# Optimization experiments

Measured on AMD Instinct MI355X. Metric: run time of the kernel, lower is better.

## Reference

```python
import jax, jax.numpy as jnp
import numpy as np

N = 50000      # nodes
E = 800000     # edges
H = 64         # hid_dim (== in_dim)
T = 4          # number of S2V message-passing steps


def setup_inputs() -> dict:
    key = jax.random.key(0)
    ks = jax.random.split(key, 12)
    mu = jax.random.normal(ks[0], (N, H), dtype=jnp.float32)
    x = jax.random.uniform(ks[1], (N, 1), dtype=jnp.float32)
    edge_index = jax.random.randint(ks[2], (2, E), 0, N, dtype=jnp.int64)
    edge_w = jax.random.uniform(ks[3], (E, 1), dtype=jnp.float32)
    s = 0.05  # small init scale to keep activations bounded across T relu layers
    W1 = jax.random.normal(ks[4], (T, H, 1), dtype=jnp.float32) * s   # lin1 per layer, torch [out,in]
    W2 = jax.random.normal(ks[5], (T, H, H), dtype=jnp.float32) * s   # lin2 per layer
    W3 = jax.random.normal(ks[6], (T, H, H), dtype=jnp.float32) * s   # lin3 per layer
    W4 = jax.random.normal(ks[7], (T, H, 1), dtype=jnp.float32) * s   # lin4 per layer
    W5 = jax.random.normal(ks[8], (1, 2 * H), dtype=jnp.float32) * s  # lin5
    W7 = jax.random.normal(ks[9], (H, H), dtype=jnp.float32) * s      # lin7
    return {"mu": mu, "x": x, "edge_index": edge_index, "edge_w": edge_w,
            "W1": W1, "W2": W2, "W3": W3, "W4": W4, "W5": W5, "W7": W7}


def _s2v_step(mu, x, idx, edge_w, w1, w2, w3, w4):
    # Faithful to source: gather AND scatter both use edge_index[1].
    x_emb = x @ w1.T                                            # [N,H]
    mu_j = mu[idx]                                              # [E,H] gather
    mu_aggr = jax.ops.segment_sum(mu_j, idx, num_segments=N)    # [N,H] scatter_add
    mu_aggr = mu_aggr @ w2.T
    ew = jax.nn.relu(edge_w @ w4.T)                             # [E,H]
    ew_aggr = jax.ops.segment_sum(ew, idx, num_segments=N)      # [N,H]
    ew_aggr = ew_aggr @ w3.T
    return jax.nn.relu(x_emb + mu_aggr + ew_aggr)


def reference(mu, x, edge_index, edge_w, W1, W2, W3, W4, W5, W7):
    idx = edge_index[1]
    for t in range(T):
        mu = _s2v_step(mu, x, idx, edge_w, W1[t], W2[t], W3[t], W4[t])
    nodes_vec = mu @ W7.T                                       # [N,H]
    graph_pool = jnp.broadcast_to(jnp.sum(mu, axis=0, keepdims=True), (N, H))
    cat = jnp.concatenate([graph_pool, nodes_vec], axis=1)      # [N,2H]
    return (jax.nn.relu(cat) @ W5.T).squeeze(-1)                # [N]
```

## Files before the change

kernel.cpp:

```cpp
#include <hip/hip_runtime.h>

#define H 64
#define NPB 64
#define KS 104
typedef short bf16x8 __attribute__((ext_vector_type(8)));
typedef float f32x4 __attribute__((ext_vector_type(4)));

static __device__ __forceinline__ unsigned short f2bf(float f) {
    union { float f; unsigned u; } v; v.f = f;
    unsigned r = v.u + 0x7fffu + ((v.u >> 16) & 1u);
    return (unsigned short)(r >> 16);
}
static __device__ __forceinline__ float bf2f(unsigned short b) {
    union { unsigned u; float f; } v; v.u = ((unsigned)b) << 16;
    return v.f;
}
static __device__ __forceinline__ void split8(const float* ff, bf16x8& hi, bf16x8& lo) {
#pragma unroll
    for (int j = 0; j < 8; ++j) {
        unsigned short h = f2bf(ff[j]);
        hi[j] = (short)h;
        lo[j] = (short)f2bf(ff[j] - bf2f(h));
    }
}


__global__ __launch_bounds__(256)
void prep_kernel(const float* __restrict__ W1, const float* __restrict__ W2,
                 const float* __restrict__ W3, const float* __restrict__ W4,
                 const float* __restrict__ W7, unsigned* __restrict__ zero_base,
                 int zero_dwords, bf16x8* __restrict__ Bp, bf16x8* __restrict__ W7p) {
    const int t = threadIdx.x;
    if (blockIdx.x != 0) {
        int idx = (blockIdx.x - 1) * 256 + t;
        for (int i = idx; i < zero_dwords; i += 64 * 256) zero_base[i] = 0u;
        return;
    }
    __shared__ float v3s[4 * H];
    {
        int tl = t >> 6, h = t & 63;
        const float* __restrict__ w3r = W3 + (tl * H + h) * H;
        const float* __restrict__ w4r = W4 + tl * H;
        float a0 = 0, a1 = 0, a2 = 0, a3 = 0;
#pragma unroll
        for (int k = 0; k < H; k += 4) {
            a0 += fmaxf(w4r[k + 0], 0.f) * w3r[k + 0];
            a1 += fmaxf(w4r[k + 1], 0.f) * w3r[k + 1];
            a2 += fmaxf(w4r[k + 2], 0.f) * w3r[k + 2];
            a3 += fmaxf(w4r[k + 3], 0.f) * w3r[k + 3];
        }
        v3s[t] = (a0 + a1) + (a2 + a3);
    }
    __syncthreads();
    const int w = t >> 6, lane = t & 63, c = lane & 15, q = lane >> 4;
    const int hh = 16 * w + c;
    for (int tl = 0; tl < 4; ++tl) {
        const int b3 = (tl * 4 + w) * 3;
        bf16x8 hi, lo;
#pragma unroll
        for (int s = 0; s < 2; ++s) {
            const float* __restrict__ wp = W2 + (tl * H + hh) * H + s * 32 + q * 8;
            float4 f0 = *(const float4*)(wp);
            float4 f1 = *(const float4*)(wp + 4);
            float ff[8] = {f0.x, f0.y, f0.z, f0.w, f1.x, f1.y, f1.z, f1.w};
            split8(ff, hi, lo);
            Bp[(b3 + s) * 128 + lane] = hi;
            Bp[(b3 + s) * 128 + 64 + lane] = lo;
        }
        float ff[8] = {0, 0, 0, 0, 0, 0, 0, 0};
        if (q == 0) { ff[0] = W1[tl * H + hh]; ff[1] = v3s[tl * H + hh]; }
        split8(ff, hi, lo);
        Bp[(b3 + 2) * 128 + lane] = hi;
        Bp[(b3 + 2) * 128 + 64 + lane] = lo;
    }
#pragma unroll
    for (int s = 0; s < 2; ++s) {
        const float* __restrict__ wp = W7 + hh * H + s * 32 + q * 8;
        float4 f0 = *(const float4*)(wp);
        float4 f1 = *(const float4*)(wp + 4);
        float ff[8] = {f0.x, f0.y, f0.z, f0.w, f1.x, f1.y, f1.z, f1.w};
        bf16x8 hi, lo;
        split8(ff, hi, lo);
        W7p[(w * 2 + s) * 128 + lane] = hi;
        W7p[(w * 2 + s) * 128 + 64 + lane] = lo;
    }
}

__global__ __launch_bounds__(256)
void edge_kernel(const int* __restrict__ ei, const float* __restrict__ ew,
                 double* __restrict__ dS, int E) {
    int probe = ei[2 * (threadIdx.x & 63) + 1];
    bool is64 = (__ballot(probe != 0) == 0ULL);
    int e0 = 4 * (blockIdx.x * blockDim.x + threadIdx.x);
    if (e0 >= E) return;
    if (e0 + 3 < E) {
        float4 wv = *(const float4*)(ew + e0);
        int i0, i1, i2, i3;
        if (is64) {
            int4 a = *(const int4*)(ei + 2 * (E + e0));
            int4 b = *(const int4*)(ei + 2 * (E + e0) + 4);
            i0 = a.x; i1 = a.z; i2 = b.x; i3 = b.z;
        } else {
            int4 a = *(const int4*)(ei + E + e0);
            i0 = a.x; i1 = a.y; i2 = a.z; i3 = a.w;
        }
        unsafeAtomicAdd(&dS[i0], 4096.0 + (double)wv.x);
        unsafeAtomicAdd(&dS[i1], 4096.0 + (double)wv.y);
        unsafeAtomicAdd(&dS[i2], 4096.0 + (double)wv.z);
        unsafeAtomicAdd(&dS[i3], 4096.0 + (double)wv.w);
    } else {
        for (int j = 0; j < 4 && e0 + j < E; ++j) {
            int e = e0 + j;
            int idx = is64 ? ei[2 * (E + e)] : ei[E + e];
            unsafeAtomicAdd(&dS[idx], 4096.0 + (double)ew[e]);
        }
    }
}

__global__ __launch_bounds__(256, 2)
void node_kernel(const float* __restrict__ mu, const float* __restrict__ x,
                 const float* __restrict__ W5, const bf16x8* __restrict__ Bp,
                 const bf16x8* __restrict__ W7p, const double* __restrict__ dS,
                 float* __restrict__ gp, float* __restrict__ out, int N) {
    __shared__ unsigned short Ab[2][NPB * KS];
    __shared__ float degs[NPB];
    __shared__ float red[4 * NPB];

    const int t = threadIdx.x;
    const int lane = t & 63;
    const int w = __builtin_amdgcn_readfirstlane(t >> 6);
    const int c = lane & 15;
    const int q = lane >> 4;
    const int hh = 16 * w + c;
    const int base = blockIdx.x * NPB;

    if (t < 128) {
        int buf = t >> 6, row = t & 63;
        unsigned* p = (unsigned*)&Ab[buf][row * KS];
#pragma unroll
        for (int d = 33; d < 52; ++d) p[d] = 0u;
    }
    if (t < 64) {
        int node = base + t;
        float dg = 0.f, sv = 0.f, xv = 0.f;
        if (node < N) {
            double T = dS[node];
            double k = floor(T * (1.0 / 4096.0));
            dg = (float)k;
            sv = (float)(T - 4096.0 * k);
            xv = x[node];
        }
        degs[t] = dg;
        unsigned short xb = f2bf(xv), sb = f2bf(sv);
        Ab[0][t * KS + 64] = xb; Ab[0][t * KS + 65] = sb;
        Ab[1][t * KS + 64] = xb; Ab[1][t * KS + 65] = sb;
    }
    __syncthreads();

    {
        const float* __restrict__ mublk = mu + (size_t)base * H;
        const int maxf = (N - base) * H;
#pragma unroll
        for (int cc = 0; cc < 4; ++cc) {
            int f = (t + 256 * cc) * 4;
            float4 v = make_float4(0.f, 0.f, 0.f, 0.f);
            if (f < maxf) v = *(const float4*)(mublk + f);
            int m = f >> 6, k = f & 63;
            float dg = degs[m];
            ushort4 b;
            b.x = f2bf(v.x * dg); b.y = f2bf(v.y * dg);
            b.z = f2bf(v.z * dg); b.w = f2bf(v.w * dg);
            *(ushort4*)(&Ab[0][m * KS + k]) = b;
        }
    }
    __syncthreads();

    unsigned short* Acur = &Ab[0][0];
    unsigned short* Anxt = &Ab[1][0];

    for (int tl = 0; tl < 4; ++tl) {
        const int b3 = (tl * 4 + w) * 3;
        bf16x8 bh0 = Bp[(b3 + 0) * 128 + lane], bl0 = Bp[(b3 + 0) * 128 + 64 + lane];
        bf16x8 bh1 = Bp[(b3 + 1) * 128 + lane], bl1 = Bp[(b3 + 1) * 128 + 64 + lane];
        bf16x8 bh2 = Bp[(b3 + 2) * 128 + lane], bl2 = Bp[(b3 + 2) * 128 + 64 + lane];

        f32x4 acc[4];
#pragma unroll
        for (int mt = 0; mt < 4; ++mt)
#pragma unroll
            for (int r = 0; r < 4; ++r) acc[mt][r] = 0.f;

#pragma unroll
        for (int mt = 0; mt < 4; ++mt) {
            const unsigned short* ar = Acur + (mt * 16 + c) * KS;
            bf16x8 a0 = *(const bf16x8*)(ar + q * 8);
            bf16x8 a1 = *(const bf16x8*)(ar + 32 + q * 8);
            bf16x8 a2 = *(const bf16x8*)(ar + 64 + q * 8);
            acc[mt] = __builtin_amdgcn_mfma_f32_16x16x32_bf16(a0, bh0, acc[mt], 0, 0, 0);
            acc[mt] = __builtin_amdgcn_mfma_f32_16x16x32_bf16(a0, bl0, acc[mt], 0, 0, 0);
            acc[mt] = __builtin_amdgcn_mfma_f32_16x16x32_bf16(a1, bh1, acc[mt], 0, 0, 0);
            acc[mt] = __builtin_amdgcn_mfma_f32_16x16x32_bf16(a1, bl1, acc[mt], 0, 0, 0);
            acc[mt] = __builtin_amdgcn_mfma_f32_16x16x32_bf16(a2, bh2, acc[mt], 0, 0, 0);
            acc[mt] = __builtin_amdgcn_mfma_f32_16x16x32_bf16(a2, bl2, acc[mt], 0, 0, 0);
        }

        const bool scale = (tl < 3);
#pragma unroll
        for (int mt = 0; mt < 4; ++mt) {
#pragma unroll
            for (int r = 0; r < 4; ++r) {
                int m = mt * 16 + q * 4 + r;
                float v = fmaxf(acc[mt][r], 0.f);
                if (scale) v *= degs[m];
                Anxt[m * KS + hh] = f2bf(v);
            }
        }
        __syncthreads();
        unsigned short* tmp = Acur; Acur = Anxt; Anxt = tmp;
    }

    {
        bf16x8 bh0 = W7p[(w * 2 + 0) * 128 + lane], bl0 = W7p[(w * 2 + 0) * 128 + 64 + lane];
        bf16x8 bh1 = W7p[(w * 2 + 1) * 128 + lane], bl1 = W7p[(w * 2 + 1) * 128 + 64 + lane];
        f32x4 acc[4];
#pragma unroll
        for (int mt = 0; mt < 4; ++mt)
#pragma unroll
            for (int r = 0; r < 4; ++r) acc[mt][r] = 0.f;
#pragma unroll
        for (int mt = 0; mt < 4; ++mt) {
            const unsigned short* ar = Acur + (mt * 16 + c) * KS;
            bf16x8 a0 = *(const bf16x8*)(ar + q * 8);
            bf16x8 a1 = *(const bf16x8*)(ar + 32 + q * 8);
            acc[mt] = __builtin_amdgcn_mfma_f32_16x16x32_bf16(a0, bh0, acc[mt], 0, 0, 0);
            acc[mt] = __builtin_amdgcn_mfma_f32_16x16x32_bf16(a0, bl0, acc[mt], 0, 0, 0);
            acc[mt] = __builtin_amdgcn_mfma_f32_16x16x32_bf16(a1, bh1, acc[mt], 0, 0, 0);
            acc[mt] = __builtin_amdgcn_mfma_f32_16x16x32_bf16(a1, bl1, acc[mt], 0, 0, 0);
        }
        float w5v = W5[H + hh];
#pragma unroll
        for (int mt = 0; mt < 4; ++mt) {
#pragma unroll
            for (int r = 0; r < 4; ++r) {
                float v = fmaxf(acc[mt][r], 0.f) * w5v;
                v += __shfl_xor(v, 1);
                v += __shfl_xor(v, 2);
                v += __shfl_xor(v, 4);
                v += __shfl_xor(v, 8);
                if (c == 0) red[w * 64 + mt * 16 + q * 4 + r] = v;
            }
        }
    }
    __syncthreads();
    if (t < 64) {
        float pn = red[t] + red[64 + t] + red[128 + t] + red[192 + t];
        if (base + t < N) out[base + t] = pn;
    }
    __syncthreads();

    {
        int h = t & 63, mq = t >> 6;
        float s = 0.f;
#pragma unroll
        for (int i = 0; i < 16; ++i) s += bf2f(Acur[(mq * 16 + i) * KS + h]);
        red[t] = s;
    }
    __syncthreads();
    if (t < 64) {
        float g = red[t] + red[64 + t] + red[128 + t] + red[192 + t];
        unsafeAtomicAdd(&gp[t], g);
    }
}

__global__ __launch_bounds__(256)
void finalize_kernel(const float* __restrict__ gp, const float* __restrict__ W5,
                     float* __restrict__ out, int N) {
    int lane = threadIdx.x & 63;
    float v = fmaxf(gp[lane], 0.f) * W5[lane];
    v += __shfl_xor(v, 1);
    v += __shfl_xor(v, 2);
    v += __shfl_xor(v, 4);
    v += __shfl_xor(v, 8);
    v += __shfl_xor(v, 16);
    v += __shfl_xor(v, 32);
    int n = blockIdx.x * blockDim.x + threadIdx.x;
    if (n < N) out[n] += v;
}

extern "C" void kernel_launch(void* const* d_in, const int* in_sizes, int n_in,
                              void* d_out, int out_size, void* d_ws, size_t ws_size,
                              hipStream_t stream) {
    const float* mu = (const float*)d_in[0];
    const float* x  = (const float*)d_in[1];
    const int*   ei = (const int*)d_in[2];
    const float* ew = (const float*)d_in[3];
    const float* W1 = (const float*)d_in[4];
    const float* W2 = (const float*)d_in[5];
    const float* W3 = (const float*)d_in[6];
    const float* W4 = (const float*)d_in[7];
    const float* W5 = (const float*)d_in[8];
    const float* W7 = (const float*)d_in[9];
    float* out = (float*)d_out;

    const int N = in_sizes[1];
    const int E = in_sizes[3];

    char* ws = (char*)d_ws;
    double* dS  = (double*)ws;
    float*  gp  = (float*)(ws + (size_t)N * 8);
    bf16x8* Bp  = (bf16x8*)(ws + (size_t)N * 8 + 256);
    bf16x8* W7p = (bf16x8*)(ws + (size_t)N * 8 + 256 + 196608);
    int zero_dwords = N * 2 + 64;

    prep_kernel<<<65, 256, 0, stream>>>(W1, W2, W3, W4, W7, (unsigned*)dS,
                                        zero_dwords, Bp, W7p);
    edge_kernel<<<(E + 1023) / 1024, 256, 0, stream>>>(ei, ew, dS, E);
    node_kernel<<<(N + NPB - 1) / NPB, 256, 0, stream>>>(mu, x, W5, Bp, W7p,
                                                         dS, gp, out, N);
    finalize_kernel<<<(N + 255) / 256, 256, 0, stream>>>(gp, W5, out, N);
}
```

Measured before the change: 150.2 us.

## Fuse prep, edge, node and finalize kernels into one cooperative persistent kernel

Replaces the four-kernel launch sequence with a single cooperative kernel that uses grid-wide syncs between phases: zeroing, weight packing plus edge atomics, persistent node-tile processing, and the final graph-pool add. The grid is sized from occupancy and capped at 768 blocks, and blocks loop over node tiles. This removes three launch boundaries and their inter-kernel gaps. In exchange it adds grid.sync overhead, reserves one block for weight prep during the edge phase, and depends on the cooperative-launch occupancy being valid at launch_bounds(256,3).

```diff
diff --git a/kernel.cpp b/kernel.cpp
--- a/kernel.cpp
+++ b/kernel.cpp
@@ -1,4 +1,6 @@
 #include <hip/hip_runtime.h>
+#include <hip/hip_cooperative_groups.h>
+namespace cg = cooperative_groups;
 
 #define H 64
 #define NPB 64
@@ -24,115 +26,114 @@
     }
 }
 
-
-__global__ __launch_bounds__(256)
-void prep_kernel(const float* __restrict__ W1, const float* __restrict__ W2,
-                 const float* __restrict__ W3, const float* __restrict__ W4,
-                 const float* __restrict__ W7, unsigned* __restrict__ zero_base,
-                 int zero_dwords, bf16x8* __restrict__ Bp, bf16x8* __restrict__ W7p) {
-    const int t = threadIdx.x;
-    if (blockIdx.x != 0) {
-        int idx = (blockIdx.x - 1) * 256 + t;
-        for (int i = idx; i < zero_dwords; i += 64 * 256) zero_base[i] = 0u;
-        return;
-    }
-    __shared__ float v3s[4 * H];
-    {
-        int tl = t >> 6, h = t & 63;
-        const float* __restrict__ w3r = W3 + (tl * H + h) * H;
-        const float* __restrict__ w4r = W4 + tl * H;
-        float a0 = 0, a1 = 0, a2 = 0, a3 = 0;
-#pragma unroll
-        for (int k = 0; k < H; k += 4) {
-            a0 += fmaxf(w4r[k + 0], 0.f) * w3r[k + 0];
-            a1 += fmaxf(w4r[k + 1], 0.f) * w3r[k + 1];
-            a2 += fmaxf(w4r[k + 2], 0.f) * w3r[k + 2];
-            a3 += fmaxf(w4r[k + 3], 0.f) * w3r[k + 3];
-        }
-        v3s[t] = (a0 + a1) + (a2 + a3);
-    }
-    __syncthreads();
-    const int w = t >> 6, lane = t & 63, c = lane & 15, q = lane >> 4;
-    const int hh = 16 * w + c;
-    for (int tl = 0; tl < 4; ++tl) {
-        const int b3 = (tl * 4 + w) * 3;
-        bf16x8 hi, lo;
-#pragma unroll
-        for (int s = 0; s < 2; ++s) {
-            const float* __restrict__ wp = W2 + (tl * H + hh) * H + s * 32 + q * 8;
-            float4 f0 = *(const float4*)(wp);
-            float4 f1 = *(const float4*)(wp + 4);
-            float ff[8] = {f0.x, f0.y, f0.z, f0.w, f1.x, f1.y, f1.z, f1.w};
-            split8(ff, hi, lo);
-            Bp[(b3 + s) * 128 + lane] = hi;
-            Bp[(b3 + s) * 128 + 64 + lane] = lo;
-        }
-        float ff[8] = {0, 0, 0, 0, 0, 0, 0, 0};
-        if (q == 0) { ff[0] = W1[tl * H + hh]; ff[1] = v3s[tl * H + hh]; }
-        split8(ff, hi, lo);
-        Bp[(b3 + 2) * 128 + lane] = hi;
-        Bp[(b3 + 2) * 128 + 64 + lane] = lo;
-    }
-#pragma unroll
-    for (int s = 0; s < 2; ++s) {
-        const float* __restrict__ wp = W7 + hh * H + s * 32 + q * 8;
-        float4 f0 = *(const float4*)(wp);
-        float4 f1 = *(const float4*)(wp + 4);
-        float ff[8] = {f0.x, f0.y, f0.z, f0.w, f1.x, f1.y, f1.z, f1.w};
-        bf16x8 hi, lo;
-        split8(ff, hi, lo);
-        W7p[(w * 2 + s) * 128 + lane] = hi;
-        W7p[(w * 2 + s) * 128 + 64 + lane] = lo;
-    }
-}
-
-__global__ __launch_bounds__(256)
-void edge_kernel(const int* __restrict__ ei, const float* __restrict__ ew,
-                 double* __restrict__ dS, int E) {
-    int probe = ei[2 * (threadIdx.x & 63) + 1];
-    bool is64 = (__ballot(probe != 0) == 0ULL);
-    int e0 = 4 * (blockIdx.x * blockDim.x + threadIdx.x);
-    if (e0 >= E) return;
-    if (e0 + 3 < E) {
-        float4 wv = *(const float4*)(ew + e0);
-        int i0, i1, i2, i3;
-        if (is64) {
-            int4 a = *(const int4*)(ei + 2 * (E + e0));
-            int4 b = *(const int4*)(ei + 2 * (E + e0) + 4);
-            i0 = a.x; i1 = a.z; i2 = b.x; i3 = b.z;
-        } else {
-            int4 a = *(const int4*)(ei + E + e0);
-            i0 = a.x; i1 = a.y; i2 = a.z; i3 = a.w;
-        }
-        unsafeAtomicAdd(&dS[i0], 4096.0 + (double)wv.x);
-        unsafeAtomicAdd(&dS[i1], 4096.0 + (double)wv.y);
-        unsafeAtomicAdd(&dS[i2], 4096.0 + (double)wv.z);
-        unsafeAtomicAdd(&dS[i3], 4096.0 + (double)wv.w);
-    } else {
-        for (int j = 0; j < 4 && e0 + j < E; ++j) {
-            int e = e0 + j;
-            int idx = is64 ? ei[2 * (E + e)] : ei[E + e];
-            unsafeAtomicAdd(&dS[idx], 4096.0 + (double)ew[e]);
-        }
-    }
-}
-
-__global__ __launch_bounds__(256, 2)
-void node_kernel(const float* __restrict__ mu, const float* __restrict__ x,
-                 const float* __restrict__ W5, const bf16x8* __restrict__ Bp,
-                 const bf16x8* __restrict__ W7p, const double* __restrict__ dS,
-                 float* __restrict__ gp, float* __restrict__ out, int N) {
+__global__ __launch_bounds__(256, 3)
+void fused_kernel(const float* __restrict__ mu, const float* __restrict__ x,
+                  const int* __restrict__ ei, const float* __restrict__ ew,
+                  const float* __restrict__ W1, const float* __restrict__ W2,
+                  const float* __restrict__ W3, const float* __restrict__ W4,
+                  const float* __restrict__ W5, const float* __restrict__ W7,
+                  double* __restrict__ dS, float* __restrict__ gp,
+                  bf16x8* __restrict__ Bp, bf16x8* __restrict__ W7p,
+                  float* __restrict__ out, int N, int E) {
+    cg::grid_group grid = cg::this_grid();
     __shared__ unsigned short Ab[2][NPB * KS];
     __shared__ float degs[NPB];
-    __shared__ float red[4 * NPB];
+    __shared__ float red[256];
+    __shared__ float v3s[256];
 
     const int t = threadIdx.x;
+    const int bid = blockIdx.x;
+    const int nb = gridDim.x;
     const int lane = t & 63;
     const int w = __builtin_amdgcn_readfirstlane(t >> 6);
     const int c = lane & 15;
     const int q = lane >> 4;
     const int hh = 16 * w + c;
-    const int base = blockIdx.x * NPB;
+
+    {
+        unsigned* zb = (unsigned*)dS;
+        const int zd = 2 * N;
+        for (int i = bid * 256 + t; i < zd; i += nb * 256) zb[i] = 0u;
+        if (bid == 0 && t < 64) gp[t] = 0.f;
+    }
+    grid.sync();
+
+    if (bid == 0) {
+        {
+            int tl = t >> 6, h2 = t & 63;
+            const float* __restrict__ w3r = W3 + (tl * H + h2) * H;
+            const float* __restrict__ w4r = W4 + tl * H;
+            float a0 = 0, a1 = 0, a2 = 0, a3 = 0;
+#pragma unroll
+            for (int k = 0; k < H; k += 4) {
+                a0 += fmaxf(w4r[k + 0], 0.f) * w3r[k + 0];
+                a1 += fmaxf(w4r[k + 1], 0.f) * w3r[k + 1];
+                a2 += fmaxf(w4r[k + 2], 0.f) * w3r[k + 2];
+                a3 += fmaxf(w4r[k + 3], 0.f) * w3r[k + 3];
+            }
+            v3s[t] = (a0 + a1) + (a2 + a3);
+        }
+        __syncthreads();
+        for (int tl = 0; tl < 4; ++tl) {
+            const int b3 = (tl * 4 + w) * 3;
+            bf16x8 hi, lo;
+#pragma unroll
+            for (int s = 0; s < 2; ++s) {
+                const float* __restrict__ wp = W2 + (tl * H + hh) * H + s * 32 + q * 8;
+                float4 f0 = *(const float4*)(wp);
+                float4 f1 = *(const float4*)(wp + 4);
+                float ff[8] = {f0.x, f0.y, f0.z, f0.w, f1.x, f1.y, f1.z, f1.w};
+                split8(ff, hi, lo);
+                Bp[(b3 + s) * 128 + lane] = hi;
+                Bp[(b3 + s) * 128 + 64 + lane] = lo;
+            }
+            float ff[8] = {0, 0, 0, 0, 0, 0, 0, 0};
+            if (q == 0) { ff[0] = W1[tl * H + hh]; ff[1] = v3s[tl * H + hh]; }
+            split8(ff, hi, lo);
+            Bp[(b3 + 2) * 128 + lane] = hi;
+            Bp[(b3 + 2) * 128 + 64 + lane] = lo;
+        }
+#pragma unroll
+        for (int s = 0; s < 2; ++s) {
+            const float* __restrict__ wp = W7 + hh * H + s * 32 + q * 8;
+            float4 f0 = *(const float4*)(wp);
+            float4 f1 = *(const float4*)(wp + 4);
+            float ff[8] = {f0.x, f0.y, f0.z, f0.w, f1.x, f1.y, f1.z, f1.w};
+            bf16x8 hi, lo;
+            split8(ff, hi, lo);
+            W7p[(w * 2 + s) * 128 + lane] = hi;
+            W7p[(w * 2 + s) * 128 + 64 + lane] = lo;
+        }
+    } else {
+        int probe = ei[2 * (t & 63) + 1];
+        bool is64 = (__ballot(probe != 0) == 0ULL);
+        const int nth = (nb - 1) * 256;
+        for (int e0 = 4 * ((bid - 1) * 256 + t); e0 < E; e0 += 4 * nth) {
+            if (e0 + 3 < E) {
+                float4 wv = *(const float4*)(ew + e0);
+                int i0, i1, i2, i3;
+                if (is64) {
+                    int4 a = *(const int4*)(ei + 2 * (E + e0));
+                    int4 b = *(const int4*)(ei + 2 * (E + e0) + 4);
+                    i0 = a.x; i1 = a.z; i2 = b.x; i3 = b.z;
+                } else {
+                    int4 a = *(const int4*)(ei + E + e0);
+                    i0 = a.x; i1 = a.y; i2 = a.z; i3 = a.w;
+                }
+                unsafeAtomicAdd(&dS[i0], 4096.0 + (double)wv.x);
+                unsafeAtomicAdd(&dS[i1], 4096.0 + (double)wv.y);
+                unsafeAtomicAdd(&dS[i2], 4096.0 + (double)wv.z);
+                unsafeAtomicAdd(&dS[i3], 4096.0 + (double)wv.w);
+            } else {
+                for (int j = 0; j < 4 && e0 + j < E; ++j) {
+                    int e = e0 + j;
+                    int idx = is64 ? ei[2 * (E + e)] : ei[E + e];
+                    unsafeAtomicAdd(&dS[idx], 4096.0 + (double)ew[e]);
+                }
+            }
+        }
+    }
+    grid.sync();
 
     if (t < 128) {
         int buf = t >> 6, row = t & 63;
@@ -140,151 +141,154 @@
 #pragma unroll
         for (int d = 33; d < 52; ++d) p[d] = 0u;
     }
-    if (t < 64) {
-        int node = base + t;
-        float dg = 0.f, sv = 0.f, xv = 0.f;
-        if (node < N) {
-            double T = dS[node];
-            double k = floor(T * (1.0 / 4096.0));
-            dg = (float)k;
-            sv = (float)(T - 4096.0 * k);
-            xv = x[node];
-        }
-        degs[t] = dg;
-        unsigned short xb = f2bf(xv), sb = f2bf(sv);
-        Ab[0][t * KS + 64] = xb; Ab[0][t * KS + 65] = sb;
-        Ab[1][t * KS + 64] = xb; Ab[1][t * KS + 65] = sb;
-    }
-    __syncthreads();
+    const int ntiles = (N + NPB - 1) / NPB;
+    for (int tile = bid; tile < ntiles; tile += nb) {
+        const int base = tile * NPB;
+
+        if (t < 64) {
+            int node = base + t;
+            float dg = 0.f, sv = 0.f, xv = 0.f;
+            if (node < N) {
+                double T = dS[node];
+                double k = floor(T * (1.0 / 4096.0));
+                dg = (float)k;
+                sv = (float)(T - 4096.0 * k);
+                xv = x[node];
+            }
+            degs[t] = dg;
+            unsigned short xb = f2bf(xv), sb = f2bf(sv);
+            Ab[0][t * KS + 64] = xb; Ab[0][t * KS + 65] = sb;
+            Ab[1][t * KS + 64] = xb; Ab[1][t * KS + 65] = sb;
+        }
+        __syncthreads();
+
+        {
+            const float* __restrict__ mublk = mu + (size_t)base * H;
+            const int maxf = (N - base) * H;
+#pragma unroll
+            for (int cc = 0; cc < 4; ++cc) {
+                int f = (t + 256 * cc) * 4;
+                float4 v = make_float4(0.f, 0.f, 0.f, 0.f);
+                if (f < maxf) v = *(const float4*)(mublk + f);
+                int m = f >> 6, k = f & 63;
+                float dg = degs[m];
+                ushort4 b;
+                b.x = f2bf(v.x * dg); b.y = f2bf(v.y * dg);
+                b.z = f2bf(v.z * dg); b.w = f2bf(v.w * dg);
+                *(ushort4*)(&Ab[0][m * KS + k]) = b;
+            }
+        }
+        __syncthreads();
+
+        unsigned short* Acur = &Ab[0][0];
+        unsigned short* Anxt = &Ab[1][0];
+
+        for (int tl = 0; tl < 4; ++tl) {
+            const int b3 = (tl * 4 + w) * 3;
+            bf16x8 bh0 = Bp[(b3 + 0) * 128 + lane], bl0 = Bp[(b3 + 0) * 128 + 64 + lane];
+            bf16x8 bh1 = Bp[(b3 + 1) * 128 + lane], bl1 = Bp[(b3 + 1) * 128 + 64 + lane];
+            bf16x8 bh2 = Bp[(b3 + 2) * 128 + lane], bl2 = Bp[(b3 + 2) * 128 + 64 + lane];
+
+            f32x4 acc[4];
+#pragma unroll
+            for (int mt = 0; mt < 4; ++mt)
+#pragma unroll
+                for (int r = 0; r < 4; ++r) acc[mt][r] = 0.f;
+
+#pragma unroll
+            for (int mt = 0; mt < 4; ++mt) {
+                const unsigned short* ar = Acur + (mt * 16 + c) * KS;
+                bf16x8 a0 = *(const bf16x8*)(ar + q * 8);
+                bf16x8 a1 = *(const bf16x8*)(ar + 32 + q * 8);
+                bf16x8 a2 = *(const bf16x8*)(ar + 64 + q * 8);
+                acc[mt] = __builtin_amdgcn_mfma_f32_16x16x32_bf16(a0, bh0, acc[mt], 0, 0, 0);
+                acc[mt] = __builtin_amdgcn_mfma_f32_16x16x32_bf16(a0, bl0, acc[mt], 0, 0, 0);
+                acc[mt] = __builtin_amdgcn_mfma_f32_16x16x32_bf16(a1, bh1, acc[mt], 0, 0, 0);
+                acc[mt] = __builtin_amdgcn_mfma_f32_16x16x32_bf16(a1, bl1, acc[mt], 0, 0, 0);
+                acc[mt] = __builtin_amdgcn_mfma_f32_16x16x32_bf16(a2, bh2, acc[mt], 0, 0, 0);
+                acc[mt] = __builtin_amdgcn_mfma_f32_16x16x32_bf16(a2, bl2, acc[mt], 0, 0, 0);
+            }
+
+            const bool scale = (tl < 3);
+#pragma unroll
+            for (int mt = 0; mt < 4; ++mt) {
+#pragma unroll
+                for (int r = 0; r < 4; ++r) {
+                    int m = mt * 16 + q * 4 + r;
+                    float v = fmaxf(acc[mt][r], 0.f);
+                    if (scale) v *= degs[m];
+                    Anxt[m * KS + hh] = f2bf(v);
+                }
+            }
+            __syncthreads();
+            unsigned short* tmp = Acur; Acur = Anxt; Anxt = tmp;
+        }
+
+        {
+            bf16x8 bh0 = W7p[(w * 2 + 0) * 128 + lane], bl0 = W7p[(w * 2 + 0) * 128 + 64 + lane];
+            bf16x8 bh1 = W7p[(w * 2 + 1) * 128 + lane], bl1 = W7p[(w * 2 + 1) * 128 + 64 + lane];
+            f32x4 acc[4];
+#pragma unroll
+            for (int mt = 0; mt < 4; ++mt)
+#pragma unroll
+                for (int r = 0; r < 4; ++r) acc[mt][r] = 0.f;
+#pragma unroll
+            for (int mt = 0; mt < 4; ++mt) {
+                const unsigned short* ar = Acur + (mt * 16 + c) * KS;
+                bf16x8 a0 = *(const bf16x8*)(ar + q * 8);
+                bf16x8 a1 = *(const bf16x8*)(ar + 32 + q * 8);
+                acc[mt] = __builtin_amdgcn_mfma_f32_16x16x32_bf16(a0, bh0, acc[mt], 0, 0, 0);
+                acc[mt] = __builtin_amdgcn_mfma_f32_16x16x32_bf16(a0, bl0, acc[mt], 0, 0, 0);
+                acc[mt] = __builtin_amdgcn_mfma_f32_16x16x32_bf16(a1, bh1, acc[mt], 0, 0, 0);
+                acc[mt] = __builtin_amdgcn_mfma_f32_16x16x32_bf16(a1, bl1, acc[mt], 0, 0, 0);
+            }
+            float w5v = W5[H + hh];
+#pragma unroll
+            for (int mt = 0; mt < 4; ++mt) {
+#pragma unroll
+                for (int r = 0; r < 4; ++r) {
+                    float v = fmaxf(acc[mt][r], 0.f) * w5v;
+                    v += __shfl_xor(v, 1);
+                    v += __shfl_xor(v, 2);
+                    v += __shfl_xor(v, 4);
+                    v += __shfl_xor(v, 8);
+                    if (c == 0) red[w * 64 + mt * 16 + q * 4 + r] = v;
+                }
+            }
+        }
+        __syncthreads();
+        if (t < 64) {
+            float pn = red[t] + red[64 + t] + red[128 + t] + red[192 + t];
+            if (base + t < N) out[base + t] = pn;
+        }
+        __syncthreads();
+
+        {
+            int h2 = t & 63, mq = t >> 6;
+            float s = 0.f;
+#pragma unroll
+            for (int i = 0; i < 16; ++i) s += bf2f(Acur[(mq * 16 + i) * KS + h2]);
+            red[t] = s;
+        }
+        __syncthreads();
+        if (t < 64) {
+            float g = red[t] + red[64 + t] + red[128 + t] + red[192 + t];
+            unsafeAtomicAdd(&gp[t], g);
+        }
+        __syncthreads();
+    }
+    grid.sync();
 
     {
-        const float* __restrict__ mublk = mu + (size_t)base * H;
-        const int maxf = (N - base) * H;
-#pragma unroll
-        for (int cc = 0; cc < 4; ++cc) {
-            int f = (t + 256 * cc) * 4;
-            float4 v = make_float4(0.f, 0.f, 0.f, 0.f);
-            if (f < maxf) v = *(const float4*)(mublk + f);
-            int m = f >> 6, k = f & 63;
-            float dg = degs[m];
-            ushort4 b;
-            b.x = f2bf(v.x * dg); b.y = f2bf(v.y * dg);
-            b.z = f2bf(v.z * dg); b.w = f2bf(v.w * dg);
-            *(ushort4*)(&Ab[0][m * KS + k]) = b;
-        }
-    }
-    __syncthreads();
-
-    unsigned short* Acur = &Ab[0][0];
-    unsigned short* Anxt = &Ab[1][0];
-
-    for (int tl = 0; tl < 4; ++tl) {
-        const int b3 = (tl * 4 + w) * 3;
-        bf16x8 bh0 = Bp[(b3 + 0) * 128 + lane], bl0 = Bp[(b3 + 0) * 128 + 64 + lane];
-        bf16x8 bh1 = Bp[(b3 + 1) * 128 + lane], bl1 = Bp[(b3 + 1) * 128 + 64 + lane];
-        bf16x8 bh2 = Bp[(b3 + 2) * 128 + lane], bl2 = Bp[(b3 + 2) * 128 + 64 + lane];
-
-        f32x4 acc[4];
-#pragma unroll
-        for (int mt = 0; mt < 4; ++mt)
-#pragma unroll
-            for (int r = 0; r < 4; ++r) acc[mt][r] = 0.f;
-
-#pragma unroll
-        for (int mt = 0; mt < 4; ++mt) {
-            const unsigned short* ar = Acur + (mt * 16 + c) * KS;
-            bf16x8 a0 = *(const bf16x8*)(ar + q * 8);
-            bf16x8 a1 = *(const bf16x8*)(ar + 32 + q * 8);
-            bf16x8 a2 = *(const bf16x8*)(ar + 64 + q * 8);
-            acc[mt] = __builtin_amdgcn_mfma_f32_16x16x32_bf16(a0, bh0, acc[mt], 0, 0, 0);
-            acc[mt] = __builtin_amdgcn_mfma_f32_16x16x32_bf16(a0, bl0, acc[mt], 0, 0, 0);
-            acc[mt] = __builtin_amdgcn_mfma_f32_16x16x32_bf16(a1, bh1, acc[mt], 0, 0, 0);
-            acc[mt] = __builtin_amdgcn_mfma_f32_16x16x32_bf16(a1, bl1, acc[mt], 0, 0, 0);
-            acc[mt] = __builtin_amdgcn_mfma_f32_16x16x32_bf16(a2, bh2, acc[mt], 0, 0, 0);
-            acc[mt] = __builtin_amdgcn_mfma_f32_16x16x32_bf16(a2, bl2, acc[mt], 0, 0, 0);
-        }
-
-        const bool scale = (tl < 3);
-#pragma unroll
-        for (int mt = 0; mt < 4; ++mt) {
-#pragma unroll
-            for (int r = 0; r < 4; ++r) {
-                int m = mt * 16 + q * 4 + r;
-                float v = fmaxf(acc[mt][r], 0.f);
-                if (scale) v *= degs[m];
-                Anxt[m * KS + hh] = f2bf(v);
-            }
-        }
-        __syncthreads();
-        unsigned short* tmp = Acur; Acur = Anxt; Anxt = tmp;
-    }
-
-    {
-        bf16x8 bh0 = W7p[(w * 2 + 0) * 128 + lane], bl0 = W7p[(w * 2 + 0) * 128 + 64 + lane];
-        bf16x8 bh1 = W7p[(w * 2 + 1) * 128 + lane], bl1 = W7p[(w * 2 + 1) * 128 + 64 + lane];
-        f32x4 acc[4];
-#pragma unroll
-        for (int mt = 0; mt < 4; ++mt)
-#pragma unroll
-            for (int r = 0; r < 4; ++r) acc[mt][r] = 0.f;
-#pragma unroll
-        for (int mt = 0; mt < 4; ++mt) {
-            const unsigned short* ar = Acur + (mt * 16 + c) * KS;
-            bf16x8 a0 = *(const bf16x8*)(ar + q * 8);
-            bf16x8 a1 = *(const bf16x8*)(ar + 32 + q * 8);
-            acc[mt] = __builtin_amdgcn_mfma_f32_16x16x32_bf16(a0, bh0, acc[mt], 0, 0, 0);
-            acc[mt] = __builtin_amdgcn_mfma_f32_16x16x32_bf16(a0, bl0, acc[mt], 0, 0, 0);
-            acc[mt] = __builtin_amdgcn_mfma_f32_16x16x32_bf16(a1, bh1, acc[mt], 0, 0, 0);
-            acc[mt] = __builtin_amdgcn_mfma_f32_16x16x32_bf16(a1, bl1, acc[mt], 0, 0, 0);
-        }
-        float w5v = W5[H + hh];
-#pragma unroll
-        for (int mt = 0; mt < 4; ++mt) {
-#pragma unroll
-            for (int r = 0; r < 4; ++r) {
-                float v = fmaxf(acc[mt][r], 0.f) * w5v;
-                v += __shfl_xor(v, 1);
-                v += __shfl_xor(v, 2);
-                v += __shfl_xor(v, 4);
-                v += __shfl_xor(v, 8);
-                if (c == 0) red[w * 64 + mt * 16 + q * 4 + r] = v;
-            }
-        }
-    }
-    __syncthreads();
-    if (t < 64) {
-        float pn = red[t] + red[64 + t] + red[128 + t] + red[192 + t];
-        if (base + t < N) out[base + t] = pn;
-    }
-    __syncthreads();
-
-    {
-        int h = t & 63, mq = t >> 6;
-        float s = 0.f;
-#pragma unroll
-        for (int i = 0; i < 16; ++i) s += bf2f(Acur[(mq * 16 + i) * KS + h]);
-        red[t] = s;
-    }
-    __syncthreads();
-    if (t < 64) {
-        float g = red[t] + red[64 + t] + red[128 + t] + red[192 + t];
-        unsafeAtomicAdd(&gp[t], g);
-    }
-}
-
-__global__ __launch_bounds__(256)
-void finalize_kernel(const float* __restrict__ gp, const float* __restrict__ W5,
-                     float* __restrict__ out, int N) {
-    int lane = threadIdx.x & 63;
-    float v = fmaxf(gp[lane], 0.f) * W5[lane];
-    v += __shfl_xor(v, 1);
-    v += __shfl_xor(v, 2);
-    v += __shfl_xor(v, 4);
-    v += __shfl_xor(v, 8);
-    v += __shfl_xor(v, 16);
-    v += __shfl_xor(v, 32);
-    int n = blockIdx.x * blockDim.x + threadIdx.x;
-    if (n < N) out[n] += v;
+        float v = fmaxf(gp[lane], 0.f) * W5[lane];
+        v += __shfl_xor(v, 1);
+        v += __shfl_xor(v, 2);
+        v += __shfl_xor(v, 4);
+        v += __shfl_xor(v, 8);
+        v += __shfl_xor(v, 16);
+        v += __shfl_xor(v, 32);
+        for (int n = bid * 256 + t; n < N; n += nb * 256) out[n] += v;
+    }
 }
 
 extern "C" void kernel_launch(void* const* d_in, const int* in_sizes, int n_in,
@@ -302,20 +306,23 @@
     const float* W7 = (const float*)d_in[9];
     float* out = (float*)d_out;
 
-    const int N = in_sizes[1];
-    const int E = in_sizes[3];
+    int N = in_sizes[1];
+    int E = in_sizes[3];
 
     char* ws = (char*)d_ws;
     double* dS  = (double*)ws;
     float*  gp  = (float*)(ws + (size_t)N * 8);
     bf16x8* Bp  = (bf16x8*)(ws + (size_t)N * 8 + 256);
     bf16x8* W7p = (bf16x8*)(ws + (size_t)N * 8 + 256 + 196608);
-    int zero_dwords = N * 2 + 64;
-
-    prep_kernel<<<65, 256, 0, stream>>>(W1, W2, W3, W4, W7, (unsigned*)dS,
-                                        zero_dwords, Bp, W7p);
-    edge_kernel<<<(E + 1023) / 1024, 256, 0, stream>>>(ei, ew, dS, E);
-    node_kernel<<<(N + NPB - 1) / NPB, 256, 0, stream>>>(mu, x, W5, Bp, W7p,
-                                                         dS, gp, out, N);
-    finalize_kernel<<<(N + 255) / 256, 256, 0, stream>>>(gp, W5, out, N);
-}
+
+    int maxb = 0;
+    hipOccupancyMaxActiveBlocksPerMultiprocessor(&maxb, fused_kernel, 256, 0);
+    if (maxb < 1) maxb = 1;
+    int nb = maxb * 256;
+    if (nb > 768) nb = 768;
+
+    void* args[] = {&mu, &x, &ei, &ew, &W1, &W2, &W3, &W4, &W5, &W7,
+                    &dS, &gp, &Bp, &W7p, &out, &N, &E};
+    hipLaunchCooperativeKernel((void*)fused_kernel, dim3(nb), dim3(256),
+                               args, 0, stream);
+}
```

Measured after the change: 289.8 us. 92.9% more time.

## Merge weight prep into edge kernel and pack degree/weight sums in fp32

Applied to the files above, without the earlier changes.

Weight preprocessing now runs in block 0 of the edge-scatter kernel instead of in a separate launch. The workspace zeroing moves to hipMemsetAsync. The packed degree-plus-weight-sum accumulator changes from fp64 atomics to fp32 atomics, which halves atomic traffic but lowers the precision of the recovered edge-weight sum. Each edge thread now handles eight edges, and node_kernel's launch bounds ask for four blocks per CU, which risks register pressure or spills.

```diff
diff --git a/kernel.cpp b/kernel.cpp
--- a/kernel.cpp
+++ b/kernel.cpp
@@ -26,101 +26,101 @@
 
 
 __global__ __launch_bounds__(256)
-void prep_kernel(const float* __restrict__ W1, const float* __restrict__ W2,
-                 const float* __restrict__ W3, const float* __restrict__ W4,
-                 const float* __restrict__ W7, unsigned* __restrict__ zero_base,
-                 int zero_dwords, bf16x8* __restrict__ Bp, bf16x8* __restrict__ W7p) {
+void edge_prep_kernel(const int* __restrict__ ei, const float* __restrict__ ew,
+                      const float* __restrict__ W1, const float* __restrict__ W2,
+                      const float* __restrict__ W3, const float* __restrict__ W4,
+                      const float* __restrict__ W7, float* __restrict__ dSf,
+                      bf16x8* __restrict__ Bp, bf16x8* __restrict__ W7p, int E) {
+    __shared__ float v3s[256];
     const int t = threadIdx.x;
-    if (blockIdx.x != 0) {
-        int idx = (blockIdx.x - 1) * 256 + t;
-        for (int i = idx; i < zero_dwords; i += 64 * 256) zero_base[i] = 0u;
-        return;
-    }
-    __shared__ float v3s[4 * H];
-    {
-        int tl = t >> 6, h = t & 63;
-        const float* __restrict__ w3r = W3 + (tl * H + h) * H;
-        const float* __restrict__ w4r = W4 + tl * H;
-        float a0 = 0, a1 = 0, a2 = 0, a3 = 0;
-#pragma unroll
-        for (int k = 0; k < H; k += 4) {
-            a0 += fmaxf(w4r[k + 0], 0.f) * w3r[k + 0];
-            a1 += fmaxf(w4r[k + 1], 0.f) * w3r[k + 1];
-            a2 += fmaxf(w4r[k + 2], 0.f) * w3r[k + 2];
-            a3 += fmaxf(w4r[k + 3], 0.f) * w3r[k + 3];
-        }
-        v3s[t] = (a0 + a1) + (a2 + a3);
-    }
-    __syncthreads();
-    const int w = t >> 6, lane = t & 63, c = lane & 15, q = lane >> 4;
-    const int hh = 16 * w + c;
-    for (int tl = 0; tl < 4; ++tl) {
-        const int b3 = (tl * 4 + w) * 3;
-        bf16x8 hi, lo;
+    const int bid = blockIdx.x;
+
+    if (bid == 0) {
+        {
+            int tl = t >> 6, h2 = t & 63;
+            const float* __restrict__ w3r = W3 + (tl * H + h2) * H;
+            const float* __restrict__ w4r = W4 + tl * H;
+            float a0 = 0, a1 = 0, a2 = 0, a3 = 0;
+#pragma unroll
+            for (int k = 0; k < H; k += 4) {
+                a0 += fmaxf(w4r[k + 0], 0.f) * w3r[k + 0];
+                a1 += fmaxf(w4r[k + 1], 0.f) * w3r[k + 1];
+                a2 += fmaxf(w4r[k + 2], 0.f) * w3r[k + 2];
+                a3 += fmaxf(w4r[k + 3], 0.f) * w3r[k + 3];
+            }
+            v3s[t] = (a0 + a1) + (a2 + a3);
+        }
+        __syncthreads();
+        const int w = t >> 6, lane = t & 63, c = lane & 15, q = lane >> 4;
+        const int hh = 16 * w + c;
+        for (int tl = 0; tl < 4; ++tl) {
+            const int b3 = (tl * 4 + w) * 3;
+            bf16x8 hi, lo;
+#pragma unroll
+            for (int s = 0; s < 2; ++s) {
+                const float* __restrict__ wp = W2 + (tl * H + hh) * H + s * 32 + q * 8;
+                float4 f0 = *(const float4*)(wp);
+                float4 f1 = *(const float4*)(wp + 4);
+                float ff[8] = {f0.x, f0.y, f0.z, f0.w, f1.x, f1.y, f1.z, f1.w};
+                split8(ff, hi, lo);
+                Bp[(b3 + s) * 128 + lane] = hi;
+                Bp[(b3 + s) * 128 + 64 + lane] = lo;
+            }
+            float ff[8] = {0, 0, 0, 0, 0, 0, 0, 0};
+            if (q == 0) { ff[0] = W1[tl * H + hh]; ff[1] = v3s[tl * H + hh]; }
+            split8(ff, hi, lo);
+            Bp[(b3 + 2) * 128 + lane] = hi;
+            Bp[(b3 + 2) * 128 + 64 + lane] = lo;
+        }
 #pragma unroll
         for (int s = 0; s < 2; ++s) {
-            const float* __restrict__ wp = W2 + (tl * H + hh) * H + s * 32 + q * 8;
+            const float* __restrict__ wp = W7 + hh * H + s * 32 + q * 8;
             float4 f0 = *(const float4*)(wp);
             float4 f1 = *(const float4*)(wp + 4);
             float ff[8] = {f0.x, f0.y, f0.z, f0.w, f1.x, f1.y, f1.z, f1.w};
+            bf16x8 hi, lo;
             split8(ff, hi, lo);
-            Bp[(b3 + s) * 128 + lane] = hi;
-            Bp[(b3 + s) * 128 + 64 + lane] = lo;
-        }
-        float ff[8] = {0, 0, 0, 0, 0, 0, 0, 0};
-        if (q == 0) { ff[0] = W1[tl * H + hh]; ff[1] = v3s[tl * H + hh]; }
-        split8(ff, hi, lo);
-        Bp[(b3 + 2) * 128 + lane] = hi;
-        Bp[(b3 + 2) * 128 + 64 + lane] = lo;
-    }
-#pragma unroll
-    for (int s = 0; s < 2; ++s) {
-        const float* __restrict__ wp = W7 + hh * H + s * 32 + q * 8;
-        float4 f0 = *(const float4*)(wp);
-        float4 f1 = *(const float4*)(wp + 4);
-        float ff[8] = {f0.x, f0.y, f0.z, f0.w, f1.x, f1.y, f1.z, f1.w};
-        bf16x8 hi, lo;
-        split8(ff, hi, lo);
-        W7p[(w * 2 + s) * 128 + lane] = hi;
-        W7p[(w * 2 + s) * 128 + 64 + lane] = lo;
-    }
-}
-
-__global__ __launch_bounds__(256)
-void edge_kernel(const int* __restrict__ ei, const float* __restrict__ ew,
-                 double* __restrict__ dS, int E) {
-    int probe = ei[2 * (threadIdx.x & 63) + 1];
+            W7p[(w * 2 + s) * 128 + lane] = hi;
+            W7p[(w * 2 + s) * 128 + 64 + lane] = lo;
+        }
+        return;
+    }
+
+    int probe = ei[2 * (t & 63) + 1];
     bool is64 = (__ballot(probe != 0) == 0ULL);
-    int e0 = 4 * (blockIdx.x * blockDim.x + threadIdx.x);
-    if (e0 >= E) return;
-    if (e0 + 3 < E) {
-        float4 wv = *(const float4*)(ew + e0);
-        int i0, i1, i2, i3;
-        if (is64) {
-            int4 a = *(const int4*)(ei + 2 * (E + e0));
-            int4 b = *(const int4*)(ei + 2 * (E + e0) + 4);
-            i0 = a.x; i1 = a.z; i2 = b.x; i3 = b.z;
+    const int base_e = 8 * ((bid - 1) * 256 + t);
+#pragma unroll
+    for (int g = 0; g < 2; ++g) {
+        int e0 = base_e + 4 * g;
+        if (e0 + 3 < E) {
+            float4 wv = *(const float4*)(ew + e0);
+            int i0, i1, i2, i3;
+            if (is64) {
+                int4 a = *(const int4*)(ei + 2 * (E + e0));
+                int4 b = *(const int4*)(ei + 2 * (E + e0) + 4);
+                i0 = a.x; i1 = a.z; i2 = b.x; i3 = b.z;
+            } else {
+                int4 a = *(const int4*)(ei + E + e0);
+                i0 = a.x; i1 = a.y; i2 = a.z; i3 = a.w;
+            }
+            unsafeAtomicAdd(&dSf[i0], 4096.0f + wv.x);
+            unsafeAtomicAdd(&dSf[i1], 4096.0f + wv.y);
+            unsafeAtomicAdd(&dSf[i2], 4096.0f + wv.z);
+            unsafeAtomicAdd(&dSf[i3], 4096.0f + wv.w);
         } else {
-            int4 a = *(const int4*)(ei + E + e0);
-            i0 = a.x; i1 = a.y; i2 = a.z; i3 = a.w;
-        }
-        unsafeAtomicAdd(&dS[i0], 4096.0 + (double)wv.x);
-        unsafeAtomicAdd(&dS[i1], 4096.0 + (double)wv.y);
-        unsafeAtomicAdd(&dS[i2], 4096.0 + (double)wv.z);
-        unsafeAtomicAdd(&dS[i3], 4096.0 + (double)wv.w);
-    } else {
-        for (int j = 0; j < 4 && e0 + j < E; ++j) {
-            int e = e0 + j;
-            int idx = is64 ? ei[2 * (E + e)] : ei[E + e];
-            unsafeAtomicAdd(&dS[idx], 4096.0 + (double)ew[e]);
-        }
-    }
-}
-
-__global__ __launch_bounds__(256, 2)
+            for (int j = 0; j < 4 && e0 + j < E; ++j) {
+                int e = e0 + j;
+                int idx = is64 ? ei[2 * (E + e)] : ei[E + e];
+                unsafeAtomicAdd(&dSf[idx], 4096.0f + ew[e]);
+            }
+        }
+    }
+}
+
+__global__ __launch_bounds__(256, 4)
 void node_kernel(const float* __restrict__ mu, const float* __restrict__ x,
                  const float* __restrict__ W5, const bf16x8* __restrict__ Bp,
-                 const bf16x8* __restrict__ W7p, const double* __restrict__ dS,
+                 const bf16x8* __restrict__ W7p, const float* __restrict__ dSf,
                  float* __restrict__ gp, float* __restrict__ out, int N) {
     __shared__ unsigned short Ab[2][NPB * KS];
     __shared__ float degs[NPB];
@@ -144,10 +144,10 @@
         int node = base + t;
         float dg = 0.f, sv = 0.f, xv = 0.f;
         if (node < N) {
-            double T = dS[node];
-            double k = floor(T * (1.0 / 4096.0));
-            dg = (float)k;
-            sv = (float)(T - 4096.0 * k);
+            float T = dSf[node];
+            float k = floorf(T * (1.0f / 4096.0f));
+            dg = k;
+            sv = T - 4096.0f * k;
             xv = x[node];
         }
         degs[t] = dg;
@@ -259,10 +259,10 @@
     __syncthreads();
 
     {
-        int h = t & 63, mq = t >> 6;
+        int h2 = t & 63, mq = t >> 6;
         float s = 0.f;
 #pragma unroll
-        for (int i = 0; i < 16; ++i) s += bf2f(Acur[(mq * 16 + i) * KS + h]);
+        for (int i = 0; i < 16; ++i) s += bf2f(Acur[(mq * 16 + i) * KS + h2]);
         red[t] = s;
     }
     __syncthreads();
@@ -306,16 +306,17 @@
     const int E = in_sizes[3];
 
     char* ws = (char*)d_ws;
-    double* dS  = (double*)ws;
-    float*  gp  = (float*)(ws + (size_t)N * 8);
-    bf16x8* Bp  = (bf16x8*)(ws + (size_t)N * 8 + 256);
-    bf16x8* W7p = (bf16x8*)(ws + (size_t)N * 8 + 256 + 196608);
-    int zero_dwords = N * 2 + 64;
-
-    prep_kernel<<<65, 256, 0, stream>>>(W1, W2, W3, W4, W7, (unsigned*)dS,
-                                        zero_dwords, Bp, W7p);
-    edge_kernel<<<(E + 1023) / 1024, 256, 0, stream>>>(ei, ew, dS, E);
+    float*  dSf = (float*)ws;
+    float*  gp  = (float*)(ws + (size_t)N * 4);
+    bf16x8* Bp  = (bf16x8*)(ws + (size_t)N * 4 + 256);
+    bf16x8* W7p = (bf16x8*)(ws + (size_t)N * 4 + 256 + 196608);
+
+    hipMemsetAsync(ws, 0, (size_t)N * 4 + 256, stream);
+
+    int nb_e = 1 + (E + 8 * 256 - 1) / (8 * 256);
+    edge_prep_kernel<<<nb_e, 256, 0, stream>>>(ei, ew, W1, W2, W3, W4, W7,
+                                               dSf, Bp, W7p, E);
     node_kernel<<<(N + NPB - 1) / NPB, 256, 0, stream>>>(mu, x, W5, Bp, W7p,
-                                                         dS, gp, out, N);
+                                                         dSf, gp, out, N);
     finalize_kernel<<<(N + 255) / 256, 256, 0, stream>>>(gp, W5, out, N);
 }
```

New measurement: 154.5 us. +2.9%, slower.
